# Kernel tuning notes

Measured on AMD Instinct MI355X. Metric: run time of the kernel, lower is better.

Reference implementation:

```python
import jax, jax.numpy as jnp
import numpy as np

N, NH, G, SEG, RATIO = 500000, 128, 10000, 25, 2
P = G * SEG            # 250000 pos samples
PN = P * RATIO         # 500000 neg samples


def setup_inputs() -> dict:
    key = jax.random.key(0)
    k1, k2, k3, k4, k5, k6 = jax.random.split(key, 6)
    return {
        "embedding": jax.random.normal(k1, (N, NH), jnp.float32),
        "embedding_": jax.random.normal(k2, (N, NH), jnp.float32),
        "grid_sizes": jnp.full((G,), SEG, dtype=jnp.int64 if jax.config.jax_enable_x64 else jnp.int32),
        "pos_samples": jax.random.randint(k3, (P,), 0, N),
        "neg_samples": jax.random.randint(k4, (PN,), 0, N),
        "Wi": jax.random.normal(k5, (NH, NH), jnp.float32) * (1.0 / np.sqrt(NH)),
        "bi": jnp.zeros((NH,), jnp.float32),
        "Wk": jax.random.normal(k6, (NH, NH), jnp.float32) * (1.0 / np.sqrt(NH)),  # Bilinear weight [1,nh,nh] squeezed
        "bk": jnp.zeros((1,), jnp.float32),
    }


def reference(embedding, embedding_, grid_sizes, pos_samples, neg_samples, Wi, bi, Wk, bk):
    Pl = pos_samples.shape[0]
    Gl = grid_sizes.shape[0]
    ratio = neg_samples.shape[0] // Pl  # static int

    # segment ids: grid index repeated grid_sizes[i] times (sum == P)
    seg_ids = jnp.repeat(jnp.arange(Gl), grid_sizes, total_repeat_length=Pl)

    # f_i on embedding_ , gather pos, segment-mean per grid
    emb_ = embedding_ @ Wi.T + bi                      # [N, nh]
    pos_e_ = emb_[pos_samples]                         # [P, nh]
    seg_sum = jax.ops.segment_sum(pos_e_, seg_ids, num_segments=Gl)
    grid_embed = seg_sum / grid_sizes[:, None].astype(seg_sum.dtype)  # [G, nh]

    # f_i on embedding, gather pos/neg samples
    emb = embedding @ Wi.T + bi
    pos_embed = emb[pos_samples]                       # [P, nh]
    neg_embed = emb[neg_samples]                       # [P*ratio, nh]

    # broadcast grid embedding back to per-sample rows
    pos_grid = grid_embed[seg_ids]                     # [P, nh]
    neg_seg_ids = jnp.repeat(jnp.arange(Gl), grid_sizes * ratio,
                             total_repeat_length=Pl * ratio)
    neg_grid = grid_embed[neg_seg_ids]                 # [P*ratio, nh]

    # bilinear score: x1 W x2 + b (out features = 1, squeezed)
    pos_logits = jnp.einsum('nd,de,ne->n', pos_embed, Wk, pos_grid) + bk[0]
    neg_logits = jnp.einsum('nd,de,ne->n', neg_embed, Wk, neg_grid) + bk[0]
    return jnp.concatenate((pos_logits, neg_logits))
```

## Files before the change

kernel.cpp:

```cpp
#include <hip/hip_runtime.h>

#define NH 128

__global__ void scan_kernel(const int* __restrict__ gs, int* __restrict__ c, int G) {
    __shared__ int part[1024];
    int t = threadIdx.x;
    int chunk = (G + 1023) >> 10;
    int b = t * chunk;
    int e = min(b + chunk, G);
    int s = 0;
    for (int i = b; i < e; ++i) s += gs[i];
    part[t] = s;
    __syncthreads();
    for (int off = 1; off < 1024; off <<= 1) {
        int val = (t >= off) ? part[t - off] : 0;
        __syncthreads();
        part[t] += val;
        __syncthreads();
    }
    int excl = (t == 0) ? 0 : part[t - 1];
    for (int i = b; i < e; ++i) { c[i] = excl; excl += gs[i]; }
    if (t == 1023) c[G] = part[1023];
}

__global__ void matA_kernel(const float* __restrict__ Wk, const float* __restrict__ Wi,
                            const float* __restrict__ bi,
                            float* __restrict__ A, float* __restrict__ u) {
    int tid = blockIdx.x * blockDim.x + threadIdx.x;
    int e = tid >> 7, d = tid & (NH - 1);
    float acc = 0.f;
    for (int f = 0; f < NH; ++f) acc += Wk[e * NH + f] * Wi[f * NH + d];
    A[e * NH + d] = acc;
    if (tid < NH) {
        float s = 0.f;
        for (int f = 0; f < NH; ++f) s += Wk[tid * NH + f] * bi[f];
        u[tid] = s;
    }
}

__global__ void matB_kernel(const float* __restrict__ Wi, const float* __restrict__ bi,
                            const float* __restrict__ bk,
                            const float* __restrict__ A, const float* __restrict__ u,
                            float* __restrict__ Bt, float* __restrict__ v,
                            float* __restrict__ w, float* __restrict__ s0) {
    int tid = blockIdx.x * blockDim.x + threadIdx.x;
    int i = tid & (NH - 1);
    int j = tid >> 7;
    float acc = 0.f;
    for (int e = 0; e < NH; ++e) acc += Wi[e * NH + i] * A[e * NH + j];
    Bt[j * NH + i] = acc;
    if (tid < NH) {
        float s = 0.f;
        for (int e = 0; e < NH; ++e) s += Wi[e * NH + tid] * u[e];
        v[tid] = s;
    } else if (tid < 2 * NH) {
        int jj = tid - NH;
        float s = 0.f;
        for (int e = 0; e < NH; ++e) s += bi[e] * A[e * NH + jj];
        w[jj] = s;
    }
    if (tid == 0) {
        float s = 0.f;
        for (int e = 0; e < NH; ++e) s += bi[e] * u[e];
        s0[0] = s + bk[0];
    }
}

__global__ void seg_mean_kernel(const float* __restrict__ emb_, const int* __restrict__ pos,
                                const int* __restrict__ c, float* __restrict__ M, int G) {
    __shared__ float smf[8 * NH];
    int g = blockIdx.x;
    int t = threadIdx.x;
    int lane = t & 31, slot = t >> 5;
    int b = c[g], e = c[g + 1];
    float4 acc = make_float4(0.f, 0.f, 0.f, 0.f);
    for (int r = b + slot; r < e; r += 8) {
        int row = pos[r];
        const float4 a = ((const float4*)(emb_ + (size_t)row * NH))[lane];
        acc.x += a.x; acc.y += a.y; acc.z += a.z; acc.w += a.w;
    }
    ((float4*)(smf + slot * NH))[lane] = acc;
    __syncthreads();
    if (t < NH) {
        float s = 0.f;
#pragma unroll
        for (int s2 = 0; s2 < 8; ++s2) s += smf[s2 * NH + t];
        float cnt = (float)max(e - b, 1);
        M[(size_t)g * NH + t] = s / cnt;
    }
}

#define SPB 8
__global__ void q_kernel(const float* __restrict__ M, const float* __restrict__ Bt,
                         const float* __restrict__ v, const float* __restrict__ w,
                         const float* __restrict__ s0,
                         float* __restrict__ Q, float* __restrict__ C2, int G) {
    __shared__ float m[SPB][NH];
    __shared__ float red[SPB][2];
    int d = threadIdx.x;
    int g0 = blockIdx.x * SPB;
    int ns = min(SPB, G - g0);
    for (int s = 0; s < SPB; ++s)
        m[s][d] = (s < ns) ? M[(size_t)(g0 + s) * NH + d] : 0.f;
    __syncthreads();

    float q[SPB];
#pragma unroll
    for (int s = 0; s < SPB; ++s) q[s] = 0.f;
    for (int f = 0; f < NH; ++f) {
        float bt = Bt[f * NH + d];
#pragma unroll
        for (int s = 0; s < SPB; ++s) q[s] += bt * m[s][f];
    }
    float vd = v[d], wd = w[d], s00 = s0[0];
    for (int s = 0; s < ns; ++s)
        Q[(size_t)(g0 + s) * NH + d] = q[s] + vd;

    int lane = d & 63, wv = d >> 6;
    for (int s = 0; s < SPB; ++s) {
        float tval = wd * m[s][d];
        for (int off = 32; off; off >>= 1) tval += __shfl_xor(tval, off);
        if (lane == 0) red[s][wv] = tval;
    }
    __syncthreads();
    if (d < SPB && d < ns) C2[g0 + d] = red[d][0] + red[d][1] + s00;
}

__global__ void logits_kernel(const float* __restrict__ emb, const int* __restrict__ pos,
                              const int* __restrict__ neg, const int* __restrict__ c,
                              const float* __restrict__ Q, const float* __restrict__ C2,
                              float* __restrict__ out, int P, int ratio) {
    __shared__ float qs[NH];
    __shared__ int idx[512];
    int g = blockIdx.x;
    int t = threadIdx.x;
    if (t < NH) qs[t] = Q[(size_t)g * NH + t];
    int pb = c[g], pe = c[g + 1];
    int np = pe - pb;
    int nb = pb * ratio;
    int tot = np + np * ratio;
    int lane = t & 31, slot = t >> 5;
    __syncthreads();
    float4 qr = ((const float4*)qs)[lane];
    float c2 = C2[g];

    for (int k0 = 0; k0 < tot; k0 += 512) {
        int kend = min(tot - k0, 512);
        __syncthreads();
        for (int k = t; k < kend; k += 256) {
            int kk = k0 + k;
            idx[k] = (kk < np) ? pos[pb + kk] : neg[nb + kk - np];
        }
        __syncthreads();
        for (int k = slot; k < kend; k += 8) {
            int kk = k0 + k;
            int row = idx[k];
            const float4 a = ((const float4*)(emb + (size_t)row * NH))[lane];
            float val = a.x * qr.x + a.y * qr.y + a.z * qr.z + a.w * qr.w;
#pragma unroll
            for (int off = 16; off; off >>= 1) val += __shfl_xor(val, off, 32);
            if (lane == 0) {
                int o = (kk < np) ? (pb + kk) : (P + nb + kk - np);
                out[o] = val + c2;
            }
        }
    }
}

extern "C" void kernel_launch(void* const* d_in, const int* in_sizes, int n_in,
                              void* d_out, int out_size, void* d_ws, size_t ws_size,
                              hipStream_t stream) {
    const float* embedding  = (const float*)d_in[0];
    const float* embedding_ = (const float*)d_in[1];
    const int*   grid_sizes = (const int*)d_in[2];
    const int*   pos        = (const int*)d_in[3];
    const int*   neg        = (const int*)d_in[4];
    const float* Wi         = (const float*)d_in[5];
    const float* bi         = (const float*)d_in[6];
    const float* Wk         = (const float*)d_in[7];
    const float* bk         = (const float*)d_in[8];

    int G = in_sizes[2];
    int P = in_sizes[3];
    int PN = in_sizes[4];
    int ratio = PN / P;

    char* ws = (char*)d_ws;
    size_t off = 0;
    auto alloc = [&](size_t bytes) {
        void* p = ws + off;
        off += (bytes + 255) & ~(size_t)255;
        return p;
    };
    int*   c   = (int*)  alloc((size_t)(G + 1) * sizeof(int));
    float* A   = (float*)alloc(NH * NH * sizeof(float));
    float* u   = (float*)alloc(NH * sizeof(float));
    float* Bt  = (float*)alloc(NH * NH * sizeof(float));
    float* v   = (float*)alloc(NH * sizeof(float));
    float* w   = (float*)alloc(NH * sizeof(float));
    float* s0  = (float*)alloc(sizeof(float));
    float* Q   = (float*)alloc((size_t)G * NH * sizeof(float));
    float* C2  = (float*)alloc((size_t)G * sizeof(float));
    float* M   = (float*)alloc((size_t)G * NH * sizeof(float));
    (void)ws_size; (void)n_in; (void)out_size;

    hipLaunchKernelGGL(scan_kernel, dim3(1), dim3(1024), 0, stream, grid_sizes, c, G);
    hipLaunchKernelGGL(matA_kernel, dim3((NH * NH) / 256), dim3(256), 0, stream,
                       Wk, Wi, bi, A, u);
    hipLaunchKernelGGL(matB_kernel, dim3((NH * NH) / 256), dim3(256), 0, stream,
                       Wi, bi, bk, A, u, Bt, v, w, s0);
    hipLaunchKernelGGL(seg_mean_kernel, dim3(G), dim3(256), 0, stream,
                       embedding_, pos, c, M, G);
    hipLaunchKernelGGL(q_kernel, dim3((G + SPB - 1) / SPB), dim3(NH), 0, stream,
                       M, Bt, v, w, s0, Q, C2, G);
    hipLaunchKernelGGL(logits_kernel, dim3(G), dim3(256), 0, stream,
                       embedding, pos, neg, c, Q, C2, (float*)d_out, P, ratio);
}
```

Before: 541.6 us.

## Fuse segment mean with Q projection and batch logits loads and stores

```diff
diff --git a/kernel.cpp b/kernel.cpp
--- a/kernel.cpp
+++ b/kernel.cpp
@@ -66,13 +66,20 @@
     }
 }
 
-__global__ void seg_mean_kernel(const float* __restrict__ emb_, const int* __restrict__ pos,
-                                const int* __restrict__ c, float* __restrict__ M, int G) {
+__global__ void seg_q_kernel(const float* __restrict__ emb_, const int* __restrict__ pos,
+                             const int* __restrict__ c,
+                             const float* __restrict__ Bt, const float* __restrict__ v,
+                             const float* __restrict__ w, const float* __restrict__ s0,
+                             float* __restrict__ Q, float* __restrict__ C2, int G) {
     __shared__ float smf[8 * NH];
+    __shared__ float m[NH];
+    __shared__ float half_acc[2][NH];
+    __shared__ float red[2];
     int g = blockIdx.x;
     int t = threadIdx.x;
     int lane = t & 31, slot = t >> 5;
     int b = c[g], e = c[g + 1];
+
     float4 acc = make_float4(0.f, 0.f, 0.f, 0.f);
     for (int r = b + slot; r < e; r += 8) {
         int row = pos[r];
@@ -84,46 +91,31 @@
     if (t < NH) {
         float s = 0.f;
 #pragma unroll
-        for (int s2 = 0; s2 < 8; ++s2) s += smf[s2 * NH + t];
-        float cnt = (float)max(e - b, 1);
-        M[(size_t)g * NH + t] = s / cnt;
-    }
-}
-
-#define SPB 8
-__global__ void q_kernel(const float* __restrict__ M, const float* __restrict__ Bt,
-                         const float* __restrict__ v, const float* __restrict__ w,
-                         const float* __restrict__ s0,
-                         float* __restrict__ Q, float* __restrict__ C2, int G) {
-    __shared__ float m[SPB][NH];
-    __shared__ float red[SPB][2];
-    int d = threadIdx.x;
-    int g0 = blockIdx.x * SPB;
-    int ns = min(SPB, G - g0);
-    for (int s = 0; s < SPB; ++s)
-        m[s][d] = (s < ns) ? M[(size_t)(g0 + s) * NH + d] : 0.f;
-    __syncthreads();
-
-    float q[SPB];
-#pragma unroll
-    for (int s = 0; s < SPB; ++s) q[s] = 0.f;
-    for (int f = 0; f < NH; ++f) {
-        float bt = Bt[f * NH + d];
-#pragma unroll
-        for (int s = 0; s < SPB; ++s) q[s] += bt * m[s][f];
-    }
-    float vd = v[d], wd = w[d], s00 = s0[0];
-    for (int s = 0; s < ns; ++s)
-        Q[(size_t)(g0 + s) * NH + d] = q[s] + vd;
-
-    int lane = d & 63, wv = d >> 6;
-    for (int s = 0; s < SPB; ++s) {
-        float tval = wd * m[s][d];
-        for (int off = 32; off; off >>= 1) tval += __shfl_xor(tval, off);
-        if (lane == 0) red[s][wv] = tval;
-    }
-    __syncthreads();
-    if (d < SPB && d < ns) C2[g0 + d] = red[d][0] + red[d][1] + s00;
+        for (int i = 0; i < 8; ++i) s += smf[i * NH + t];
+        m[t] = s / (float)max(e - b, 1);
+    }
+    __syncthreads();
+
+    int d = t & (NH - 1);
+    int h = t >> 7;
+    int f0 = h * 64;
+    float acc2 = 0.f;
+#pragma unroll
+    for (int f = 0; f < 64; ++f)
+        acc2 += Bt[(size_t)(f0 + f) * NH + d] * m[f0 + f];
+    half_acc[h][d] = acc2;
+
+    if (t < NH) {
+        float tv = w[t] * m[t];
+#pragma unroll
+        for (int off = 32; off; off >>= 1) tv += __shfl_xor(tv, off);
+        if ((t & 63) == 0) red[t >> 6] = tv;
+    }
+    __syncthreads();
+    if (t < NH)
+        Q[(size_t)g * NH + t] = half_acc[0][t] + half_acc[1][t] + v[t];
+    if (t == 0)
+        C2[g] = red[0] + red[1] + s0[0];
 }
 
 __global__ void logits_kernel(const float* __restrict__ emb, const int* __restrict__ pos,
@@ -132,6 +124,7 @@
                               float* __restrict__ out, int P, int ratio) {
     __shared__ float qs[NH];
     __shared__ int idx[512];
+    __shared__ float res[512];
     int g = blockIdx.x;
     int t = threadIdx.x;
     if (t < NH) qs[t] = Q[(size_t)g * NH + t];
@@ -146,24 +139,39 @@
 
     for (int k0 = 0; k0 < tot; k0 += 512) {
         int kend = min(tot - k0, 512);
-        __syncthreads();
         for (int k = t; k < kend; k += 256) {
             int kk = k0 + k;
             idx[k] = (kk < np) ? pos[pb + kk] : neg[nb + kk - np];
         }
         __syncthreads();
-        for (int k = slot; k < kend; k += 8) {
-            int kk = k0 + k;
-            int row = idx[k];
-            const float4 a = ((const float4*)(emb + (size_t)row * NH))[lane];
-            float val = a.x * qr.x + a.y * qr.y + a.z * qr.z + a.w * qr.w;
-#pragma unroll
-            for (int off = 16; off; off >>= 1) val += __shfl_xor(val, off, 32);
-            if (lane == 0) {
-                int o = (kk < np) ? (pb + kk) : (P + nb + kk - np);
-                out[o] = val + c2;
+        for (int k = slot; k < kend; k += 16) {
+            int k1 = k + 8;
+            int row0 = idx[k];
+            const float4 a0 = ((const float4*)(emb + (size_t)row0 * NH))[lane];
+            float4 a1;
+            int row1 = -1;
+            if (k1 < kend) {
+                row1 = idx[k1];
+                a1 = ((const float4*)(emb + (size_t)row1 * NH))[lane];
+            }
+            float v0 = a0.x * qr.x + a0.y * qr.y + a0.z * qr.z + a0.w * qr.w;
+#pragma unroll
+            for (int off = 16; off; off >>= 1) v0 += __shfl_xor(v0, off, 32);
+            if (lane == 0) res[k] = v0 + c2;
+            if (row1 >= 0) {
+                float v1 = a1.x * qr.x + a1.y * qr.y + a1.z * qr.z + a1.w * qr.w;
+#pragma unroll
+                for (int off = 16; off; off >>= 1) v1 += __shfl_xor(v1, off, 32);
+                if (lane == 0) res[k1] = v1 + c2;
             }
         }
+        __syncthreads();
+        for (int k = t; k < kend; k += 256) {
+            int kk = k0 + k;
+            int o = (kk < np) ? (pb + kk) : (P + nb + kk - np);
+            out[o] = res[k];
+        }
+        __syncthreads();
     }
 }
 
@@ -201,7 +209,6 @@
     float* s0  = (float*)alloc(sizeof(float));
     float* Q   = (float*)alloc((size_t)G * NH * sizeof(float));
     float* C2  = (float*)alloc((size_t)G * sizeof(float));
-    float* M   = (float*)alloc((size_t)G * NH * sizeof(float));
     (void)ws_size; (void)n_in; (void)out_size;
 
     hipLaunchKernelGGL(scan_kernel, dim3(1), dim3(1024), 0, stream, grid_sizes, c, G);
@@ -209,10 +216,8 @@
                        Wk, Wi, bi, A, u);
     hipLaunchKernelGGL(matB_kernel, dim3((NH * NH) / 256), dim3(256), 0, stream,
                        Wi, bi, bk, A, u, Bt, v, w, s0);
-    hipLaunchKernelGGL(seg_mean_kernel, dim3(G), dim3(256), 0, stream,
-                       embedding_, pos, c, M, G);
-    hipLaunchKernelGGL(q_kernel, dim3((G + SPB - 1) / SPB), dim3(NH), 0, stream,
-                       M, Bt, v, w, s0, Q, C2, G);
+    hipLaunchKernelGGL(seg_q_kernel, dim3(G), dim3(256), 0, stream,
+                       embedding_, pos, c, Bt, v, w, s0, Q, C2, G);
     hipLaunchKernelGGL(logits_kernel, dim3(G), dim3(256), 0, stream,
                        embedding, pos, neg, c, Q, C2, (float*)d_out, P, ratio);
 }
```

Measured after the change: 557.0 us. 2.8% more time.
